# Kernel tuning notes

Hardware: AMD Instinct MI355X
Metric: run time of the kernel (lower is better)

## Reference

```python
import jax, jax.numpy as jnp
import numpy as np

GROUP_SIZE = 64
NUM_HEADS = 16
NUM_KV_HEADS = 4
ROPE_BASE = 10000.0


def rms_norm(x):
    eps = jnp.asarray(jnp.finfo(x.dtype).eps, x.dtype)
    return x * jax.lax.rsqrt(jnp.mean(x * x, axis=-1, keepdims=True) + eps)


def ternary_weight(w, g=GROUP_SIZE):
    # fake-quant with straight-through estimator, matching torch bf16 cast
    wb = w.astype(jnp.bfloat16)
    wg = wb.reshape(-1, g)
    scale = jnp.clip(jnp.mean(jnp.abs(wg), axis=-1, keepdims=True), 1e-8)
    q = jnp.clip(jnp.round(wg / scale), -1, 1)
    wq = (q * scale).reshape(w.shape)
    return wb + jax.lax.stop_gradient(wq - wb)


def ternary_linear(x, w):
    wt = ternary_weight(w).astype(x.dtype)
    return x @ wt.T


def apply_rotary_emb(x, cos, sin):
    half = x.shape[-1] // 2
    x1, x2 = x[..., :half], x[..., half:]
    return jnp.concatenate((x1 * cos + x2 * sin, x1 * -sin + x2 * cos), axis=-1)


def rotary_tables(seq_len, head_dim, dtype):
    inv_freq = 1.0 / (ROPE_BASE ** (jnp.arange(0, head_dim, 2, dtype=jnp.float32) / head_dim))
    freqs = jnp.outer(jnp.arange(seq_len, dtype=jnp.float32), inv_freq)  # [S, D/2]
    cos = jnp.cos(freqs)[None, :, None, :].astype(dtype)  # [1,S,1,D/2]
    sin = jnp.sin(freqs)[None, :, None, :].astype(dtype)
    return cos, sin


def setup_inputs() -> dict:
    key = jax.random.key(0)
    k1, k2, k3 = jax.random.split(key, 3)
    dim = 1024
    q_size = NUM_HEADS * (dim // NUM_HEADS)
    kv_size = NUM_KV_HEADS * (dim // NUM_HEADS)
    return {
        "x": jax.random.normal(k1, (2, 2048, dim), dtype=jnp.float32),
        "w_qkv": jax.random.normal(k2, (q_size + 2 * kv_size, dim), dtype=jnp.float32) * 0.02,
        "w_proj": jax.random.normal(k3, (dim, dim), dtype=jnp.float32) * 0.02,
        "q_gain": jnp.ones((NUM_HEADS,), dtype=jnp.float32),
    }


def reference(x, w_qkv, w_proj, q_gain):
    bsz, seqlen, dim = x.shape
    head_dim = dim // NUM_HEADS
    q_size = NUM_HEADS * head_dim
    kv_size = NUM_KV_HEADS * head_dim

    qkv = ternary_linear(x, w_qkv)
    q = qkv[..., :q_size].reshape(bsz, seqlen, NUM_HEADS, head_dim)
    k = qkv[..., q_size:q_size + kv_size].reshape(bsz, seqlen, NUM_KV_HEADS, head_dim)
    v = qkv[..., q_size + kv_size:].reshape(bsz, seqlen, NUM_KV_HEADS, head_dim)

    q, k = rms_norm(q), rms_norm(k)
    cos, sin = rotary_tables(seqlen, head_dim, q.dtype)
    q = apply_rotary_emb(q, cos, sin)
    k = apply_rotary_emb(k, cos, sin)
    q = q * q_gain.astype(q.dtype)[None, None, :, None]

    # GQA: repeat kv heads
    rep = NUM_HEADS // NUM_KV_HEADS
    kr = jnp.repeat(k, rep, axis=2)  # [B,S,H,D]
    vr = jnp.repeat(v, rep, axis=2)

    scale = 1.0 / jnp.sqrt(jnp.asarray(head_dim, q.dtype))
    scores = jnp.einsum('bqhd,bkhd->bhqk', q, kr) * scale  # [B,H,S,S]
    causal = jnp.tril(jnp.ones((seqlen, seqlen), dtype=bool))
    scores = jnp.where(causal[None, None], scores, jnp.asarray(-jnp.inf, scores.dtype))
    probs = jax.nn.softmax(scores, axis=-1)
    y = jnp.einsum('bhqk,bkhd->bqhd', probs, vr).reshape(bsz, seqlen, dim)

    # NormedTernaryLinear: rms_norm then ternary linear
    return ternary_linear(rms_norm(y), w_proj)
```

## Files before the change

kernel.cpp:

```cpp
#include <hip/hip_runtime.h>
#include <cstdint>

typedef unsigned short u16;
typedef __bf16 bf16x8 __attribute__((ext_vector_type(8)));
typedef short s16x4 __attribute__((ext_vector_type(4)));
typedef int s32x2 __attribute__((ext_vector_type(2)));
typedef float f32x4 __attribute__((ext_vector_type(4)));

__device__ __forceinline__ u16 f2bf(float f) {
    unsigned u = __float_as_uint(f);
    u = (u + 0x7fffu + ((u >> 16) & 1u)) >> 16;
    return (u16)u;
}
__device__ __forceinline__ float bf2f(u16 h) {
    return __uint_as_float(((unsigned)h) << 16);
}

__device__ __forceinline__ void glds16(const u16* g, u16* l) {
    __builtin_amdgcn_global_load_lds(
        (const __attribute__((address_space(1))) void*)g,
        (__attribute__((address_space(3))) void*)l, 16, 0, 0);
}

__device__ __forceinline__ s16x4 pack_bf4(float p0, float p1, float p2, float p3) {
    unsigned a0 = __float_as_uint(p0) + 0x8000u;
    unsigned a1 = __float_as_uint(p1) + 0x8000u;
    unsigned a2 = __float_as_uint(p2) + 0x8000u;
    unsigned a3 = __float_as_uint(p3) + 0x8000u;
    s32x2 pk = {(int)__builtin_amdgcn_perm(a1, a0, 0x07060302u),
                (int)__builtin_amdgcn_perm(a3, a2, 0x07060302u)};
    return __builtin_bit_cast(s16x4, pk);
}

#if __has_builtin(__builtin_amdgcn_mfma_f32_16x16x16bf16_1k)
#define MFMA16(a, b, c) __builtin_amdgcn_mfma_f32_16x16x16bf16_1k(a, b, c, 0, 0, 0)
#else
static __device__ __forceinline__ f32x4 mfma16_asm(s16x4 a, s16x4 b, f32x4 c) {
    asm("v_mfma_f32_16x16x16_bf16 %0, %1, %2, %0" : "+v"(c) : "v"(a), "v"(b));
    return c;
}
#define MFMA16(a, b, c) mfma16_asm(a, b, c)
#endif

__global__ __launch_bounds__(256) void prep(
    const float* __restrict__ w_qkv, const float* __restrict__ w_proj,
    const float* __restrict__ x,
    u16* __restrict__ wqkv_b, u16* __restrict__ wproj_b, u16* __restrict__ xb) {
    int bid = blockIdx.x;
    if (bid < 1280) {
        const float* w; u16* o; size_t base;
        if (bid < 768) { w = w_qkv; o = wqkv_b; base = (size_t)bid * 2048; }
        else { w = w_proj; o = wproj_b; base = (size_t)(bid - 768) * 2048; }
        size_t i = base + (size_t)threadIdx.x * 8;
        float4 A = *(const float4*)(w + i);
        float4 B = *(const float4*)(w + i + 4);
        float wf[8] = {A.x, A.y, A.z, A.w, B.x, B.y, B.z, B.w};
        float wbf[8], ab[8];
        #pragma unroll
        for (int e = 0; e < 8; ++e) { wbf[e] = bf2f(f2bf(wf[e])); ab[e] = fabsf(wbf[e]); }
        float s = ((ab[0] + ab[1]) + (ab[2] + ab[3])) + ((ab[4] + ab[5]) + (ab[6] + ab[7]));
        s += __shfl_xor(s, 1);
        s += __shfl_xor(s, 2);
        s += __shfl_xor(s, 4);
        float scale = bf2f(f2bf(s * (1.0f / 64.0f)));
        if (scale < 1e-8f) scale = 1e-8f;
        u16 ov[8];
        #pragma unroll
        for (int e = 0; e < 8; ++e) {
            float t = bf2f(f2bf(wbf[e] / scale));
            float q = rintf(t);
            q = fminf(1.0f, fmaxf(-1.0f, q));
            float d = bf2f(f2bf(q * scale - wbf[e]));
            ov[e] = f2bf(wbf[e] + d);
        }
        *(int4*)(o + i) = *(const int4*)ov;
    } else {
        size_t i = ((size_t)(bid - 1280) * 256 + threadIdx.x) * 8;
        float4 a = *(const float4*)(x + i);
        float4 b = *(const float4*)(x + i + 4);
        u16 o[8] = {f2bf(a.x), f2bf(a.y), f2bf(a.z), f2bf(a.w),
                    f2bf(b.x), f2bf(b.y), f2bf(b.z), f2bf(b.w)};
        *(int4*)(xb + i) = *(const int4*)o;
    }
}

__global__ __launch_bounds__(256) void gemm_bt(
    const u16* __restrict__ A, const u16* __restrict__ B,
    float* __restrict__ C, int M, int N, int K) {
    __shared__ u16 As[128 * 32];
    __shared__ u16 Bs[128 * 32];
    const int tid = threadIdx.x;
    const int lane = tid & 63, w = tid >> 6;
    const int quad = lane >> 4, l16 = lane & 15;
    const int m0 = blockIdx.y * 128, n0 = blockIdx.x * 128;
    const int wm = (w >> 1) * 64, wn = (w & 1) * 64;
    const int sr_ = w * 32 + (lane >> 2);
    const int sg_ = lane & 3;
    u16* Ald = As + w * 1024 + lane * 8;
    u16* Bld = Bs + w * 1024 + lane * 8;

    f32x4 acc[4][4];
    f32x4 zero = {0.f, 0.f, 0.f, 0.f};
    #pragma unroll
    for (int i = 0; i < 4; ++i)
        #pragma unroll
        for (int j = 0; j < 4; ++j) acc[i][j] = zero;

    int aoff[4], boff[4];
    #pragma unroll
    for (int mi = 0; mi < 4; ++mi) {
        int r = wm + mi * 16 + l16;
        aoff[mi] = r * 32 + (quad ^ ((r >> 1) & 3)) * 8;
        int rb = wn + mi * 16 + l16;
        boff[mi] = rb * 32 + (quad ^ ((rb >> 1) & 3)) * 8;
    }

    for (int k0 = 0; k0 < K; k0 += 32) {
        __syncthreads();
        #pragma unroll
        for (int i = 0; i < 2; ++i) {
            int r = sr_ + i * 16;
            int g = sg_ ^ ((r >> 1) & 3);
            glds16(A + (size_t)(m0 + r) * K + k0 + g * 8, Ald + i * 512);
            glds16(B + (size_t)(n0 + r) * K + k0 + g * 8, Bld + i * 512);
        }
        __syncthreads();
        bf16x8 af[4], bfr[4];
        #pragma unroll
        for (int mi = 0; mi < 4; ++mi) af[mi]  = *(const bf16x8*)(As + aoff[mi]);
        #pragma unroll
        for (int ni = 0; ni < 4; ++ni) bfr[ni] = *(const bf16x8*)(Bs + boff[ni]);
        #pragma unroll
        for (int mi = 0; mi < 4; ++mi)
            #pragma unroll
            for (int ni = 0; ni < 4; ++ni)
                acc[mi][ni] = __builtin_amdgcn_mfma_f32_16x16x32_bf16(af[mi], bfr[ni], acc[mi][ni], 0, 0, 0);
    }
    #pragma unroll
    for (int mi = 0; mi < 4; ++mi)
        #pragma unroll
        for (int ni = 0; ni < 4; ++ni) {
            int rg = m0 + wm + mi * 16 + quad * 4;
            int cg = n0 + wn + ni * 16 + l16;
            float* cp = C + (size_t)rg * N + cg;
            #pragma unroll
            for (int r = 0; r < 4; ++r) cp[(size_t)r * N] = acc[mi][ni][r];
        }
}

__global__ __launch_bounds__(256) void fuse_qkv(
    const float* __restrict__ qkv, const float* __restrict__ gain,
    u16* __restrict__ Qb, u16* __restrict__ Kb, u16* __restrict__ Vt) {
    __shared__ u16 Vs[8][264];
    const int tid = threadIdx.x;
    const int lane = tid & 63, wid = tid >> 6;
    const int lh = lane >> 4, l16 = lane & 15;
    const int T0 = blockIdx.x * 8;
    const int dbase = l16 * 4;
    const bool hi = dbase >= 32;
    const int ibase = hi ? dbase - 32 : dbase;
    const float sgn = hi ? -1.0f : 1.0f;
    const float eps = 1.1920929e-7f;
    const float sc = 0.18033688011112042f;

    float invf[4];
    #pragma unroll
    for (int j = 0; j < 4; ++j)
        invf[j] = (float)(1.0 / pow(10000.0, (double)(ibase + j) / 32.0));

    #pragma unroll
    for (int i = 0; i < 2; ++i) {
        int tok = T0 + wid * 2 + i;
        int b = tok >> 11, s = tok & 2047;
        float cosv[4], sinv[4];
        #pragma unroll
        for (int j = 0; j < 4; ++j) {
            float fr = (float)s * invf[j];
            cosv[j] = __cosf(fr);
            sinv[j] = __sinf(fr);
        }
        const float* row = qkv + (size_t)tok * 1536;
        #pragma unroll
        for (int p = 0; p < 4; ++p) {
            int h = p * 4 + lh;
            float4 x = *(const float4*)(row + h * 64 + dbase);
            float ss = x.x * x.x + x.y * x.y + x.z * x.z + x.w * x.w;
            #pragma unroll
            for (int m = 1; m < 16; m <<= 1) ss += __shfl_xor(ss, m);
            float rn = 1.0f / sqrtf(ss * (1.0f / 64.0f) + eps);
            float xn0 = x.x * rn, xn1 = x.y * rn, xn2 = x.z * rn, xn3 = x.w * rn;
            float p0 = __shfl_xor(xn0, 8), p1 = __shfl_xor(xn1, 8);
            float p2 = __shfl_xor(xn2, 8), p3 = __shfl_xor(xn3, 8);
            float g = gain[h] * sc;
            u16 o[4] = {f2bf((xn0 * cosv[0] + sgn * p0 * sinv[0]) * g),
                        f2bf((xn1 * cosv[1] + sgn * p1 * sinv[1]) * g),
                        f2bf((xn2 * cosv[2] + sgn * p2 * sinv[2]) * g),
                        f2bf((xn3 * cosv[3] + sgn * p3 * sinv[3]) * g)};
            *(uint2*)(Qb + (((size_t)(b * 16 + h) * 2048 + s) * 64 + dbase)) = *(const uint2*)o;
        }
        {
            float4 x = *(const float4*)(row + 1024 + lh * 64 + dbase);
            float ss = x.x * x.x + x.y * x.y + x.z * x.z + x.w * x.w;
            #pragma unroll
            for (int m = 1; m < 16; m <<= 1) ss += __shfl_xor(ss, m);
            float rn = 1.0f / sqrtf(ss * (1.0f / 64.0f) + eps);
            float xn0 = x.x * rn, xn1 = x.y * rn, xn2 = x.z * rn, xn3 = x.w * rn;
            float p0 = __shfl_xor(xn0, 8), p1 = __shfl_xor(xn1, 8);
            float p2 = __shfl_xor(xn2, 8), p3 = __shfl_xor(xn3, 8);
            u16 o[4] = {f2bf(xn0 * cosv[0] + sgn * p0 * sinv[0]),
                        f2bf(xn1 * cosv[1] + sgn * p1 * sinv[1]),
                        f2bf(xn2 * cosv[2] + sgn * p2 * sinv[2]),
                        f2bf(xn3 * cosv[3] + sgn * p3 * sinv[3])};
            *(uint2*)(Kb + (((size_t)(b * 4 + lh) * 2048 + s) * 64 + dbase)) = *(const uint2*)o;
        }
        {
            float4 x = *(const float4*)(row + 1280 + lh * 64 + dbase);
            u16 o[4] = {f2bf(x.x), f2bf(x.y), f2bf(x.z), f2bf(x.w)};
            int sl = wid * 2 + i;
            *(uint2*)(&Vs[sl][lh * 64 + dbase]) = *(const uint2*)o;
        }
    }
    __syncthreads();
    {
        int kvh = tid >> 6, d = tid & 63;
        int b0 = T0 >> 11, s0 = T0 & 2047;
        u16 tmp[8];
        #pragma unroll
        for (int sl = 0; sl < 8; ++sl) tmp[sl] = Vs[sl][kvh * 64 + d];
        u16* dst = Vt + ((size_t)(b0 * 4 + kvh) * 64 + d) * 2048 + s0;
        *(int4*)(dst) = *(const int4*)(tmp);
    }
}

__global__ __launch_bounds__(512, 4) void attn(
    const u16* __restrict__ Qb, const u16* __restrict__ Kb,
    const u16* __restrict__ Vt, float* __restrict__ y,
    float* __restrict__ Opart, float2* __restrict__ ml) {
    __shared__ u16 Ks[2][64 * 64];
    __shared__ u16 Vsh[2][64 * 64];
    const int hb = blockIdx.x;
    const int h = hb & 15, b = hb >> 4, kvh = h >> 2;
    const int yid = blockIdx.y;
    int bq, c0; bool partial;
    if (yid < 16) { bq = 15 - (yid >> 1); c0 = (yid & 1) * 16; partial = true; }
    else          { bq = 23 - yid;        c0 = 0;              partial = false; }
    const int nj = partial ? (c0 ? (2 * bq - 14) : 16) : (2 * bq + 2);
    const int q0 = bq * 128;
    const int tid = threadIdx.x, lane = tid & 63, w = tid >> 6;
    const int quad = lane >> 4, l16 = lane & 15;

    const u16* Qg = Qb + ((size_t)(b * 16 + h) * 2048 + q0) * 64;
    const u16* Kg = Kb + (size_t)(b * 4 + kvh) * 2048 * 64;
    const u16* Vg = Vt + (size_t)(b * 4 + kvh) * 64 * 2048;

    const bf16x8 qa0 = *(const bf16x8*)(Qg + (size_t)(w * 16 + l16) * 64 + quad * 8);
    const bf16x8 qa1 = *(const bf16x8*)(Qg + (size_t)(w * 16 + l16) * 64 + 32 + quad * 8);

    const int sr = tid >> 3;
    const int sg = (tid & 7) ^ (sr & 7);
    u16* kd[2] = {&Ks[0][0] + tid * 8, &Ks[1][0] + tid * 8};
    u16* vd[2] = {&Vsh[0][0] + tid * 8, &Vsh[1][0] + tid * 8};

    {
        int c = (c0 + nj - 1) * 64;
        glds16(Kg + (size_t)(c + sr) * 64 + sg * 8, kd[(nj - 1) & 1]);
        glds16(Vg + (size_t)sr * 2048 + c + sg * 8, vd[(nj - 1) & 1]);
    }
    __syncthreads();

    f32x4 o[4];
    f32x4 zero = {0.f, 0.f, 0.f, 0.f};
    #pragma unroll
    for (int t = 0; t < 4; ++t) o[t] = zero;
    float m = -INFINITY, l = 0.f;

    for (int jj = nj - 1; jj >= 0; --jj) {
        if (jj > 0) {
            int c = (c0 + jj - 1) * 64;
            glds16(Kg + (size_t)(c + sr) * 64 + sg * 8, kd[(jj - 1) & 1]);
            glds16(Vg + (size_t)sr * 2048 + c + sg * 8, vd[(jj - 1) & 1]);
        }
        const u16* Kt = (jj & 1) ? &Ks[1][0] : &Ks[0][0];
        const u16* Vl = (jj & 1) ? &Vsh[1][0] : &Vsh[0][0];
        const int d = 8 * bq + w - 4 * (c0 + jj);
        if (d >= 0) {
            const int tmax = d < 3 ? d : 3;
            f32x4 st[4];
            #pragma unroll
            for (int t = 0; t < 4; ++t) {
                if (t <= tmax) {
                    int rk = t * 16 + l16;
                    bf16x8 kb0 = *(const bf16x8*)(Kt + rk * 64 + ((quad ^ (rk & 7)) * 8));
                    bf16x8 kb1 = *(const bf16x8*)(Kt + rk * 64 + (((quad + 4) ^ (rk & 7)) * 8));
                    f32x4 s = __builtin_amdgcn_mfma_f32_16x16x32_bf16(kb0, qa0, zero, 0, 0, 0);
                    s = __builtin_amdgcn_mfma_f32_16x16x32_bf16(kb1, qa1, s, 0, 0, 0);
                    if (t == d) {
                        #pragma unroll
                        for (int r = 0; r < 4; ++r)
                            if (quad * 4 + r > l16) s[r] = -1e30f;
                    }
                    st[t] = s;
                }
            }
            float mx = -1e30f;
            #pragma unroll
            for (int t = 0; t < 4; ++t)
                if (t <= tmax)
                    mx = fmaxf(mx, fmaxf(fmaxf(st[t][0], st[t][1]), fmaxf(st[t][2], st[t][3])));
            mx = fmaxf(mx, __shfl_xor(mx, 16));
            mx = fmaxf(mx, __shfl_xor(mx, 32));
            if (__any(mx > m)) {
                float mnew = fmaxf(m, mx);
                float alpha = __builtin_amdgcn_exp2f(m - mnew);
                l *= alpha;
                #pragma unroll
                for (int t = 0; t < 4; ++t) o[t] *= alpha;
                m = mnew;
            }
            float rs = 0.f;
            s16x4 pf[4];
            #pragma unroll
            for (int t = 0; t < 4; ++t) {
                if (t <= tmax) {
                    float p0 = __builtin_amdgcn_exp2f(st[t][0] - m);
                    float p1 = __builtin_amdgcn_exp2f(st[t][1] - m);
                    float p2 = __builtin_amdgcn_exp2f(st[t][2] - m);
                    float p3 = __builtin_amdgcn_exp2f(st[t][3] - m);
                    rs += (p0 + p1) + (p2 + p3);
                    pf[t] = pack_bf4(p0, p1, p2, p3);
                }
            }
            rs += __shfl_xor(rs, 16);
            rs += __shfl_xor(rs, 32);
            l += rs;
            #pragma unroll
            for (int dt = 0; dt < 4; ++dt) {
                int rv = dt * 16 + l16;
                #pragma unroll
                for (int kt = 0; kt < 4; ++kt) {
                    if (kt <= tmax) {
                        int gv = 2 * kt + (quad >> 1);
                        s16x4 va = *(const s16x4*)(Vl + rv * 64 + ((gv ^ (rv & 7)) * 8) + (quad & 1) * 4);
                        o[dt] = MFMA16(va, pf[kt], o[dt]);
                    }
                }
            }
        }
        __syncthreads();
    }

    const int q = w * 16 + l16;
    if (!partial) {
        const float inv = 1.0f / l;
        const size_t row = (size_t)b * 2048 + q0 + q;
        #pragma unroll
        for (int dt = 0; dt < 4; ++dt) {
            f32x4 a = o[dt] * inv;
            *(f32x4*)(&y[row * 1024 + h * 64 + dt * 16 + quad * 4]) = a;
        }
    } else {
        const int slot = (hb * 8 + (bq - 8)) * 2 + (c0 ? 1 : 0);
        float* Op = Opart + (size_t)slot * 8192;
        #pragma unroll
        for (int dt = 0; dt < 4; ++dt)
            *(f32x4*)(Op + q * 64 + dt * 16 + quad * 4) = o[dt];
        if (quad == 0) ml[slot * 128 + q] = make_float2(m, l);
    }
}

__global__ __launch_bounds__(256) void rmsnorm_merge(
    const float* __restrict__ y, const float* __restrict__ Opart,
    const float2* __restrict__ ml, u16* __restrict__ yb) {
    __shared__ float red[4];
    const int row = blockIdx.x, tid = threadIdx.x;
    const int b = row >> 11, s = row & 2047;
    float4 v;
    if (s < 1024) {
        v = *(const float4*)(y + (size_t)row * 1024 + tid * 4);
    } else {
        const int bq = s >> 7, q = s & 127;
        const int e = tid * 4, h = e >> 6, dh = e & 63;
        const int slot = ((b * 16 + h) * 8 + (bq - 8)) * 2;
        float2 a0 = ml[slot * 128 + q];
        float2 a1 = ml[(slot + 1) * 128 + q];
        float M = fmaxf(a0.x, a1.x);
        float w0 = __builtin_amdgcn_exp2f(a0.x - M);
        float w1 = __builtin_amdgcn_exp2f(a1.x - M);
        float inv = 1.0f / (w0 * a0.y + w1 * a1.y);
        w0 *= inv; w1 *= inv;
        const float* P0 = Opart + (size_t)slot * 8192 + q * 64 + dh;
        f32x4 x0 = *(const f32x4*)P0;
        f32x4 x1 = *(const f32x4*)(P0 + 8192);
        f32x4 r = x0 * w0 + x1 * w1;
        v.x = r[0]; v.y = r[1]; v.z = r[2]; v.w = r[3];
    }
    float ss = v.x * v.x + v.y * v.y + v.z * v.z + v.w * v.w;
    #pragma unroll
    for (int m = 1; m < 64; m <<= 1) ss += __shfl_xor(ss, m);
    if ((tid & 63) == 0) red[tid >> 6] = ss;
    __syncthreads();
    float tot = red[0] + red[1] + red[2] + red[3];
    float rn = 1.0f / sqrtf(tot * (1.0f / 1024.0f) + 1.1920929e-7f);
    u16 o[4] = {f2bf(v.x * rn), f2bf(v.y * rn), f2bf(v.z * rn), f2bf(v.w * rn)};
    *(uint2*)(yb + (size_t)row * 1024 + tid * 4) = *(const uint2*)o;
}

extern "C" void kernel_launch(void* const* d_in, const int* in_sizes, int n_in,
                              void* d_out, int out_size, void* d_ws, size_t ws_size,
                              hipStream_t stream) {
    const float* x      = (const float*)d_in[0];
    const float* w_qkv  = (const float*)d_in[1];
    const float* w_proj = (const float*)d_in[2];
    const float* q_gain = (const float*)d_in[3];
    float* out = (float*)d_out;
    char* ws = (char*)d_ws;

    u16*    wproj_b = (u16*)(ws);
    u16*    xb      = (u16*)(ws + 2097152);
    u16*    Qb      = (u16*)(ws + 2097152);
    u16*    yb      = (u16*)(ws + 2097152);
    u16*    wqkv_b  = (u16*)(ws + 10485760);
    u16*    Kb      = (u16*)(ws + 10485760);
    u16*    Vt      = (u16*)(ws + 12582912);
    float*  qkv     = (float*)(ws + 14680064);
    float*  y       = (float*)(ws + 14680064);
    float*  Opart   = (float*)(ws + 31457280);
    float2* mlb     = (float2*)(ws + 48234496);

    prep<<<3328, 256, 0, stream>>>(w_qkv, w_proj, x, wqkv_b, wproj_b, xb);
    gemm_bt<<<dim3(12, 32), 256, 0, stream>>>(xb, wqkv_b, qkv, 4096, 1536, 1024);
    fuse_qkv<<<512, 256, 0, stream>>>(qkv, q_gain, Qb, Kb, Vt);
    attn<<<dim3(32, 24), 512, 0, stream>>>(Qb, Kb, Vt, y, Opart, mlb);
    rmsnorm_merge<<<4096, 256, 0, stream>>>(y, Opart, mlb, yb);
    gemm_bt<<<dim3(8, 32), 256, 0, stream>>>(yb, wproj_b, out, 4096, 1024, 1024);
}
```

Measured before the change: 205.0 us.

## Use fixed softmax bound in attention and split-K atomics for both GEMMs

The attention kernel drops the online running-max tracking and rescaling. It subtracts a fixed per-head bound derived from the q_gain value instead, relying on the fact that RMS-normed q and k bound every score. This simplifies the split-partial merge to a plain sum divided by the summed l. Both ternary GEMMs are also split in two along K, with results accumulated through float atomics into buffers zeroed by added memsets, to raise the block count. The costs are atomic traffic, two extra memset passes, and possible exp underflow when gain magnitudes are large.

```diff
diff --git a/kernel.cpp b/kernel.cpp
--- a/kernel.cpp
+++ b/kernel.cpp
@@ -93,6 +93,7 @@
     const int lane = tid & 63, w = tid >> 6;
     const int quad = lane >> 4, l16 = lane & 15;
     const int m0 = blockIdx.y * 128, n0 = blockIdx.x * 128;
+    const int kS = blockIdx.z * (K >> 1), kE = kS + (K >> 1);
     const int wm = (w >> 1) * 64, wn = (w & 1) * 64;
     const int sr_ = w * 32 + (lane >> 2);
     const int sg_ = lane & 3;
@@ -115,7 +116,7 @@
         boff[mi] = rb * 32 + (quad ^ ((rb >> 1) & 3)) * 8;
     }
 
-    for (int k0 = 0; k0 < K; k0 += 32) {
+    for (int k0 = kS; k0 < kE; k0 += 32) {
         __syncthreads();
         #pragma unroll
         for (int i = 0; i < 2; ++i) {
@@ -144,7 +145,8 @@
             int cg = n0 + wn + ni * 16 + l16;
             float* cp = C + (size_t)rg * N + cg;
             #pragma unroll
-            for (int r = 0; r < 4; ++r) cp[(size_t)r * N] = acc[mi][ni][r];
+            for (int r = 0; r < 4; ++r)
+                unsafeAtomicAdd(cp + (size_t)r * N, acc[mi][ni][r]);
         }
 }
 
@@ -234,8 +236,8 @@
 
 __global__ __launch_bounds__(512, 4) void attn(
     const u16* __restrict__ Qb, const u16* __restrict__ Kb,
-    const u16* __restrict__ Vt, float* __restrict__ y,
-    float* __restrict__ Opart, float2* __restrict__ ml) {
+    const u16* __restrict__ Vt, const float* __restrict__ gain,
+    float* __restrict__ y, float* __restrict__ Opart, float* __restrict__ ml) {
     __shared__ u16 Ks[2][64 * 64];
     __shared__ u16 Vsh[2][64 * 64];
     const int hb = blockIdx.x;
@@ -248,6 +250,7 @@
     const int q0 = bq * 128;
     const int tid = threadIdx.x, lane = tid & 63, w = tid >> 6;
     const int quad = lane >> 4, l16 = lane & 15;
+    const float nM = -(12.0f * fabsf(gain[h]) + 1.0f);
 
     const u16* Qg = Qb + ((size_t)(b * 16 + h) * 2048 + q0) * 64;
     const u16* Kg = Kb + (size_t)(b * 4 + kvh) * 2048 * 64;
@@ -272,7 +275,7 @@
     f32x4 zero = {0.f, 0.f, 0.f, 0.f};
     #pragma unroll
     for (int t = 0; t < 4; ++t) o[t] = zero;
-    float m = -INFINITY, l = 0.f;
+    float l = 0.f;
 
     for (int jj = nj - 1; jj >= 0; --jj) {
         if (jj > 0) {
@@ -302,30 +305,15 @@
                     st[t] = s;
                 }
             }
-            float mx = -1e30f;
-            #pragma unroll
-            for (int t = 0; t < 4; ++t)
-                if (t <= tmax)
-                    mx = fmaxf(mx, fmaxf(fmaxf(st[t][0], st[t][1]), fmaxf(st[t][2], st[t][3])));
-            mx = fmaxf(mx, __shfl_xor(mx, 16));
-            mx = fmaxf(mx, __shfl_xor(mx, 32));
-            if (__any(mx > m)) {
-                float mnew = fmaxf(m, mx);
-                float alpha = __builtin_amdgcn_exp2f(m - mnew);
-                l *= alpha;
-                #pragma unroll
-                for (int t = 0; t < 4; ++t) o[t] *= alpha;
-                m = mnew;
-            }
             float rs = 0.f;
             s16x4 pf[4];
             #pragma unroll
             for (int t = 0; t < 4; ++t) {
                 if (t <= tmax) {
-                    float p0 = __builtin_amdgcn_exp2f(st[t][0] - m);
-                    float p1 = __builtin_amdgcn_exp2f(st[t][1] - m);
-                    float p2 = __builtin_amdgcn_exp2f(st[t][2] - m);
-                    float p3 = __builtin_amdgcn_exp2f(st[t][3] - m);
+                    float p0 = __builtin_amdgcn_exp2f(st[t][0] + nM);
+                    float p1 = __builtin_amdgcn_exp2f(st[t][1] + nM);
+                    float p2 = __builtin_amdgcn_exp2f(st[t][2] + nM);
+                    float p3 = __builtin_amdgcn_exp2f(st[t][3] + nM);
                     rs += (p0 + p1) + (p2 + p3);
                     pf[t] = pack_bf4(p0, p1, p2, p3);
                 }
@@ -364,13 +352,13 @@
         #pragma unroll
         for (int dt = 0; dt < 4; ++dt)
             *(f32x4*)(Op + q * 64 + dt * 16 + quad * 4) = o[dt];
-        if (quad == 0) ml[slot * 128 + q] = make_float2(m, l);
+        if (quad == 0) ml[slot * 128 + q] = l;
     }
 }
 
 __global__ __launch_bounds__(256) void rmsnorm_merge(
     const float* __restrict__ y, const float* __restrict__ Opart,
-    const float2* __restrict__ ml, u16* __restrict__ yb) {
+    const float* __restrict__ ml, u16* __restrict__ yb) {
     __shared__ float red[4];
     const int row = blockIdx.x, tid = threadIdx.x;
     const int b = row >> 11, s = row & 2047;
@@ -381,17 +369,13 @@
         const int bq = s >> 7, q = s & 127;
         const int e = tid * 4, h = e >> 6, dh = e & 63;
         const int slot = ((b * 16 + h) * 8 + (bq - 8)) * 2;
-        float2 a0 = ml[slot * 128 + q];
-        float2 a1 = ml[(slot + 1) * 128 + q];
-        float M = fmaxf(a0.x, a1.x);
-        float w0 = __builtin_amdgcn_exp2f(a0.x - M);
-        float w1 = __builtin_amdgcn_exp2f(a1.x - M);
-        float inv = 1.0f / (w0 * a0.y + w1 * a1.y);
-        w0 *= inv; w1 *= inv;
+        float l0 = ml[slot * 128 + q];
+        float l1 = ml[(slot + 1) * 128 + q];
+        float inv = 1.0f / (l0 + l1);
         const float* P0 = Opart + (size_t)slot * 8192 + q * 64 + dh;
         f32x4 x0 = *(const f32x4*)P0;
         f32x4 x1 = *(const f32x4*)(P0 + 8192);
-        f32x4 r = x0 * w0 + x1 * w1;
+        f32x4 r = (x0 + x1) * inv;
         v.x = r[0]; v.y = r[1]; v.z = r[2]; v.w = r[3];
     }
     float ss = v.x * v.x + v.y * v.y + v.z * v.z + v.w * v.w;
@@ -415,22 +399,25 @@
     float* out = (float*)d_out;
     char* ws = (char*)d_ws;
 
-    u16*    wproj_b = (u16*)(ws);
-    u16*    xb      = (u16*)(ws + 2097152);
-    u16*    Qb      = (u16*)(ws + 2097152);
-    u16*    yb      = (u16*)(ws + 2097152);
-    u16*    wqkv_b  = (u16*)(ws + 10485760);
-    u16*    Kb      = (u16*)(ws + 10485760);
-    u16*    Vt      = (u16*)(ws + 12582912);
-    float*  qkv     = (float*)(ws + 14680064);
-    float*  y       = (float*)(ws + 14680064);
-    float*  Opart   = (float*)(ws + 31457280);
-    float2* mlb     = (float2*)(ws + 48234496);
+    u16*   wproj_b = (u16*)(ws);
+    u16*   xb      = (u16*)(ws + 2097152);
+    u16*   Qb      = (u16*)(ws + 2097152);
+    u16*   yb      = (u16*)(ws + 2097152);
+    u16*   wqkv_b  = (u16*)(ws + 10485760);
+    u16*   Kb      = (u16*)(ws + 10485760);
+    u16*   Vt      = (u16*)(ws + 12582912);
+    float* qkv     = (float*)(ws + 14680064);
+    float* y       = (float*)(ws + 14680064);
+    float* Opart   = (float*)(ws + 31457280);
+    float* mlb     = (float*)(ws + 48234496);
+
+    hipMemsetAsync(qkv, 0, 25165824, stream);
+    hipMemsetAsync(out, 0, (size_t)out_size * 4, stream);
 
     prep<<<3328, 256, 0, stream>>>(w_qkv, w_proj, x, wqkv_b, wproj_b, xb);
-    gemm_bt<<<dim3(12, 32), 256, 0, stream>>>(xb, wqkv_b, qkv, 4096, 1536, 1024);
+    gemm_bt<<<dim3(12, 32, 2), 256, 0, stream>>>(xb, wqkv_b, qkv, 4096, 1536, 1024);
     fuse_qkv<<<512, 256, 0, stream>>>(qkv, q_gain, Qb, Kb, Vt);
-    attn<<<dim3(32, 24), 512, 0, stream>>>(Qb, Kb, Vt, y, Opart, mlb);
+    attn<<<dim3(32, 24), 512, 0, stream>>>(Qb, Kb, Vt, q_gain, y, Opart, mlb);
     rmsnorm_merge<<<4096, 256, 0, stream>>>(y, Opart, mlb, yb);
-    gemm_bt<<<dim3(8, 32), 256, 0, stream>>>(yb, wproj_b, out, 4096, 1024, 1024);
-}
+    gemm_bt<<<dim3(8, 32, 2), 256, 0, stream>>>(yb, wproj_b, out, 4096, 1024, 1024);
+}
```

New measurement: 245.0 us. 1.2x slower.
